# Kernel optimization log

Measured on AMD Instinct MI355X. Metric: run time of the kernel, lower is better.

## Reference

```python
import jax, jax.numpy as jnp
import numpy as np

LAM = 0.5  # self.lam_
N, T, C, H, W = 8, 8, 128, 64, 64


def setup_inputs() -> dict:
    key = jax.random.key(0)
    k1, k2, k3, k4 = jax.random.split(key, 4)
    x = jax.random.normal(k1, (N, T, C, H, W), dtype=jnp.float32)
    # Conv2d(2,1,k=3,p=1,bias=False) weights: [out=1, in=2, 3, 3]
    w_conv1 = jax.random.normal(k2, (1, 2, 3, 3), dtype=jnp.float32) * 0.1
    w_conv2 = jax.random.normal(k3, (1, 2, 3, 3), dtype=jnp.float32) * 0.1
    # Conv3d(2T, T, k=3, p=1, bias=False): [out=T, in=2T, 3, 3, 3]
    w_conv_last = jax.random.normal(k4, (T, 2 * T, 3, 3, 3), dtype=jnp.float32) * 0.05
    return {"x": x, "w_conv1": w_conv1, "w_conv2": w_conv2, "w_conv_last": w_conv_last}


def _conv2d_same(y, wgt):
    # y: [B, 2, H, W], wgt: [1, 2, 3, 3] -> [B, 1, H, W]
    return jax.lax.conv_general_dilated(
        y, wgt, window_strides=(1, 1), padding=[(1, 1), (1, 1)],
        dimension_numbers=("NCHW", "OIHW", "NCHW"))


def reference(x, w_conv1, w_conv2, w_conv_last):
    n, t, c, h, w = x.shape
    kc = int(c * LAM)
    kt = int(t * LAM)

    # pooled importance map: avg + max over spatial -> [n, t, c]
    M = jnp.mean(x, axis=(3, 4)) + jnp.max(x, axis=(3, 4))

    # --- channel top-k mask ---
    # Faithful to the torch fancy-index scatter loop: important_channels[:, i, topk_[:, i]] = 1
    # broadcasts the write over ALL batch rows, i.e. a per-timestep union over the batch.
    _, topk_c = jax.lax.top_k(M, kc)                                  # [n, t, kc]
    t_ids = jnp.broadcast_to(jnp.arange(t)[None, :, None], topk_c.shape)
    mask_ch = jnp.zeros((t, c), x.dtype).at[t_ids.ravel(), topk_c.ravel()].set(1.0)  # [t, c]

    # --- time top-k mask (on transposed map) ---
    _, topk_t = jax.lax.top_k(jnp.swapaxes(M, 1, 2), kt)              # [n, c, kt]
    c_ids = jnp.broadcast_to(jnp.arange(c)[None, :, None], topk_t.shape)
    mask_tm = jnp.zeros((c, t), x.dtype).at[c_ids.ravel(), topk_t.ravel()].set(1.0).T  # [t, c]

    # important iff (mask_ch + mask_tm)/2 == 0.5  <=> XOR of the two masks
    imp = jnp.where(mask_ch + mask_tm == 1.0, 1.0, 0.0).astype(x.dtype)  # [t, c]
    imp = imp[None, :, :, None, None]                                    # [1, t, c, 1, 1]

    im_feat = imp * x
    sub_feat = x - im_feat  # (1 - imp) * x

    im_avg = jnp.mean(im_feat, axis=2, keepdims=True) / LAM           # [n, t, 1, h, w]
    im_max = jnp.max(im_feat, axis=2, keepdims=True)
    sub_avg = jnp.mean(sub_feat, axis=2, keepdims=True) / (1.0 - LAM)
    sub_max = jnp.max(sub_feat, axis=2, keepdims=True)

    im_x = jnp.concatenate([im_avg, im_max], axis=2)                  # [n, t, 2, h, w]
    sub_x = jnp.concatenate([sub_avg, sub_max], axis=2)

    # SeqToANNContainer flattens (t, n) then conv2d per-sample; flatten order irrelevant.
    im_map = jax.nn.sigmoid(_conv2d_same(im_x.reshape(n * t, 2, h, w), w_conv1)).reshape(n, t, 1, h, w)
    sub_map = jax.nn.sigmoid(_conv2d_same(sub_x.reshape(n * t, 2, h, w), w_conv2)).reshape(n, t, 1, h, w)

    htsa = jnp.concatenate([im_map * im_feat, sub_map * sub_feat], axis=1)  # [n, 2t, c, h, w]

    # Conv3d(2t -> t, k=3, p=1): treats t as channels, c as depth
    out = jax.lax.conv_general_dilated(
        htsa, w_conv_last, window_strides=(1, 1, 1),
        padding=[(1, 1), (1, 1), (1, 1)],
        dimension_numbers=("NCDHW", "OIDHW", "NCDHW"))
    return out  # [n, t, c, h, w]
```

## Files before the change

### kernel.cpp

```cpp
#include <hip/hip_runtime.h>
#include <math.h>

#define NN 8
#define TT 8
#define CC 128
#define HH 64
#define WW 64
#define HW 4096

typedef unsigned int u32;
typedef unsigned short u16;
typedef __attribute__((ext_vector_type(8))) short short8;
typedef __attribute__((ext_vector_type(4))) float floatx4;

__device__ __forceinline__ u16 f2bf(float f){
    u32 u = __float_as_uint(f);
    u32 r = (u + 0x7fffu + ((u >> 16) & 1u)) >> 16;
    return (u16)r;
}
__device__ __forceinline__ float bf2f(u16 h){
    return __uint_as_float(((u32)h) << 16);
}

__global__ __launch_bounds__(256) void k1_M(const float* __restrict__ x, float* __restrict__ M){
    int plane = blockIdx.x * 4 + (threadIdx.x >> 6);
    int lane  = threadIdx.x & 63;
    const float* p = x + (size_t)plane * HW;
    float s = 0.f, mx = -INFINITY;
    #pragma unroll
    for (int it = 0; it < 16; ++it){
        float4 v = *(const float4*)(p + it*256 + lane*4);
        s += v.x + v.y + v.z + v.w;
        mx = fmaxf(mx, fmaxf(fmaxf(v.x, v.y), fmaxf(v.z, v.w)));
    }
    #pragma unroll
    for (int off = 32; off > 0; off >>= 1){
        s += __shfl_xor(s, off, 64);
        mx = fmaxf(mx, __shfl_xor(mx, off, 64));
    }
    if (lane == 0) M[plane] = s * (1.0f/(float)HW) + mx;
}

__global__ __launch_bounds__(128) void k2_imp(const float* __restrict__ M, float* __restrict__ imp){
    int t = blockIdx.x;
    int c = threadIdx.x;
    __shared__ float Ms[NN*CC];
    for (int n = 0; n < NN; ++n)
        Ms[n*CC + c] = M[(n*TT + t)*CC + c];
    __syncthreads();
    bool sel_ch = false;
    for (int n = 0; n < NN; ++n){
        float mv = Ms[n*CC + c];
        int rank = 0;
        for (int c2 = 0; c2 < CC; ++c2){
            float v2 = Ms[n*CC + c2];
            rank += (v2 > mv) || (v2 == mv && c2 < c);
        }
        sel_ch = sel_ch || (rank < 64);
    }
    bool sel_tm = false;
    for (int n = 0; n < NN; ++n){
        float mv = M[(n*TT + t)*CC + c];
        int rank = 0;
        for (int t2 = 0; t2 < TT; ++t2){
            float v2 = M[(n*TT + t2)*CC + c];
            rank += (v2 > mv) || (v2 == mv && t2 < t);
        }
        sel_tm = sel_tm || (rank < 4);
    }
    imp[t*CC + c] = (sel_ch != sel_tm) ? 1.0f : 0.0f;
}

__global__ __launch_bounds__(512) void k3a_stats(const float* __restrict__ x,
        const float* __restrict__ imp, u16* __restrict__ st){
    int nt = blockIdx.x; int t = nt & 7;
    int px = (blockIdx.y * 512 + threadIdx.x) * 4;
    __shared__ float ipr[CC];
    if (threadIdx.x < CC) ipr[threadIdx.x] = imp[t*CC + threadIdx.x];
    __syncthreads();
    const float* xp = x + (size_t)nt * CC * HW + px;
    float sa[4] = {0,0,0,0}, sb[4] = {0,0,0,0};
    float ma[4] = {-INFINITY,-INFINITY,-INFINITY,-INFINITY};
    float mb[4] = {-INFINITY,-INFINITY,-INFINITY,-INFINITY};
    for (int c = 0; c < CC; ++c){
        float ip = ipr[c];
        float4 v = *(const float4*)(xp + (size_t)c*HW);
        float vv[4] = {v.x, v.y, v.z, v.w};
        #pragma unroll
        for (int j = 0; j < 4; ++j){
            float a = ip*vv[j], b = vv[j] - a;
            sa[j] += a; sb[j] += b;
            ma[j] = fmaxf(ma[j], a); mb[j] = fmaxf(mb[j], b);
        }
    }
    union { u16 h[4]; uint2 v2; } o;
    #pragma unroll
    for (int j = 0; j < 4; ++j) o.h[j] = f2bf(sa[j] * (1.f/64.f));
    *(uint2*)(st + (nt*4+0)*HW + px) = o.v2;
    #pragma unroll
    for (int j = 0; j < 4; ++j) o.h[j] = f2bf(ma[j]);
    *(uint2*)(st + (nt*4+1)*HW + px) = o.v2;
    #pragma unroll
    for (int j = 0; j < 4; ++j) o.h[j] = f2bf(sb[j] * (1.f/64.f));
    *(uint2*)(st + (nt*4+2)*HW + px) = o.v2;
    #pragma unroll
    for (int j = 0; j < 4; ++j) o.h[j] = f2bf(mb[j]);
    *(uint2*)(st + (nt*4+3)*HW + px) = o.v2;
}

__global__ __launch_bounds__(256) void k3b_maps(const u16* __restrict__ st,
        const float* __restrict__ w1, const float* __restrict__ w2,
        float* __restrict__ maps){
    int nt = blockIdx.x;
    int y0 = blockIdx.y * 16;
    __shared__ float S[4*18*66];
    int tid = threadIdx.x;
    for (int idx = tid; idx < 4*18*66; idx += 256){
        int s  = idx / 1188;
        int r  = (idx % 1188) / 66;
        int xx = idx % 66;
        int gy = y0 - 1 + r, gx = xx - 1;
        float v = 0.f;
        if ((u32)gy < HH && (u32)gx < WW)
            v = bf2f(st[(nt*4 + s)*HW + gy*WW + gx]);
        S[idx] = v;
    }
    __syncthreads();
    float wa[18], wb[18];
    #pragma unroll
    for (int i = 0; i < 18; ++i){ wa[i] = w1[i]; wb[i] = w2[i]; }
    for (int k = 0; k < 4; ++k){
        int p = k*256 + tid;
        int y = p >> 6, xx = p & 63;
        float zi = 0.f, zs = 0.f;
        #pragma unroll
        for (int dy = 0; dy < 3; ++dy)
            #pragma unroll
            for (int dx = 0; dx < 3; ++dx){
                int sp = (y+dy)*66 + xx + dx;
                zi += wa[dy*3+dx] * S[sp] + wa[9+dy*3+dx] * S[1188 + sp];
                zs += wb[dy*3+dx] * S[2376 + sp] + wb[9+dy*3+dx] * S[3564 + sp];
            }
        maps[(nt*2+0)*HW + y0*WW + p] = 1.0f / (1.0f + expf(-zi));
        maps[(nt*2+1)*HW + y0*WW + p] = 1.0f / (1.0f + expf(-zs));
    }
}

__global__ __launch_bounds__(64) void kW_frag(const float* __restrict__ wlast,
        const float* __restrict__ impf, u16* __restrict__ fw){
    int c_out = blockIdx.x;
    int stp   = blockIdx.y;
    int lane  = threadIdx.x;
    int m = lane & 15, q = lane >> 4;
    int tap = 4*stp + q;
    int dc = tap / 9;
    int c_in = c_out - 1 + dc;
    bool valid = (m < 8) && (tap < 27) && ((u32)c_in < CC);
    union { u16 h[8]; uint4 v; } pk;
    #pragma unroll
    for (int j = 0; j < 8; ++j){
        float wv = 0.f;
        if (valid){
            int idx = (impf[j*CC + c_in] > 0.f) ? j : j + 8;
            wv = wlast[(m*16 + idx)*27 + tap];
        }
        pk.h[j] = f2bf(wv);
    }
    *(uint4*)(fw + (((size_t)c_out*7 + stp)*64 + lane)*8) = pk.v;
}

constexpr int offb16(int tap){
    return (((tap/9)*6 + ((tap/3)%3))*66 + (tap%3))*16;
}

__global__ __launch_bounds__(256, 6) void k5_fuse(
        const float* __restrict__ x, const float* __restrict__ impf,
        const float* __restrict__ maps, const u16* __restrict__ fw,
        float* __restrict__ out){
    __shared__ __align__(16) u16 ft[1584*8];
    __shared__ u32 mofs[4][8];
    int tid  = threadIdx.x;
    int lane = tid & 63;
    int w    = tid >> 6;
    int c0 = blockIdx.x * 2;
    int y0 = blockIdx.y * 4;
    int n  = blockIdx.z;
    int cl = w & 1;
    int c_out = c0 + cl;

    if (tid < 32){
        int cc = tid >> 3, t = tid & 7;
        int gc = c0 - 1 + cc;
        float ip = ((u32)gc < CC) ? impf[t*CC + gc] : 0.f;
        mofs[cc][t] = (u32)(((n*TT + t)*2 + (ip > 0.f ? 0 : 1)) * HW);
    }

    short8 afr[7];
    const u16* fwb = fw + ((size_t)c_out*7*64 + lane)*8;
    #pragma unroll
    for (int stp = 0; stp < 7; ++stp)
        afr[stp] = *(const short8*)(fwb + stp*512);
    __syncthreads();

    for (int idx = tid; idx < 1584; idx += 256){
        int cc  = idx / 396;
        int rm  = idx % 396;
        int yyl = rm / 66;
        int xx  = rm % 66;
        int gc = c0 - 1 + cc;
        int gy = y0 - 1 + yyl;
        int gx = xx - 1;
        uint4 v = make_uint4(0,0,0,0);
        if ((u32)gc < CC && (u32)gy < HH && (u32)gx < WW){
            int gp = gy*WW + gx;
            const float* xn = x + ((size_t)(n*TT)*CC + gc)*HW + gp;
            const float* mb = maps + gp;
            u16 hv[8];
            #pragma unroll
            for (int t = 0; t < TT; ++t){
                float xv = xn[(size_t)t*CC*HW];
                float mv = mb[mofs[cc][t]];
                hv[t] = f2bf(xv * mv);
            }
            v.x = (u32)hv[0] | ((u32)hv[1] << 16);
            v.y = (u32)hv[2] | ((u32)hv[3] << 16);
            v.z = (u32)hv[4] | ((u32)hv[5] << 16);
            v.w = (u32)hv[6] | ((u32)hv[7] << 16);
        }
        *(uint4*)(ft + idx*8) = v;
    }
    __syncthreads();

    int col = lane & 15;
    int q   = lane >> 4;
    const char* fb = (const char*)ft;
    int offs[7];
    #pragma unroll
    for (int stp = 0; stp < 7; ++stp){
        int tap = 4*stp + q;
        if (tap >= 27) tap = 0;
        offs[stp] = offb16(tap);
    }
    for (int yy = 0; yy < 2; ++yy){
        int yl = (w >> 1)*2 + yy;
        int rowb = ((cl*6 + yl)*66 + col)*16;
        #pragma unroll
        for (int xp = 0; xp < 2; ++xp){
            int b0off = rowb + xp*512;
            int b1off = b0off + 256;
            floatx4 acc0 = {0.f,0.f,0.f,0.f};
            floatx4 acc1 = {0.f,0.f,0.f,0.f};
            #pragma unroll
            for (int stp = 0; stp < 7; ++stp){
                short8 b0 = *(const short8*)(fb + b0off + offs[stp]);
                short8 b1 = *(const short8*)(fb + b1off + offs[stp]);
                acc0 = __builtin_amdgcn_mfma_f32_16x16x32_bf16(afr[stp], b0, acc0, 0, 0, 0);
                acc1 = __builtin_amdgcn_mfma_f32_16x16x32_bf16(afr[stp], b1, acc1, 0, 0, 0);
            }
            if (lane < 32){
                int y = y0 + yl;
                int xa = xp*32 + col;
                #pragma unroll
                for (int rg = 0; rg < 4; ++rg){
                    int o = (lane >> 4)*4 + rg;
                    size_t ob = (((size_t)(n*TT + o))*CC + c_out)*HW + y*WW;
                    out[ob + xa]      = acc0[rg];
                    out[ob + xa + 16] = acc1[rg];
                }
            }
        }
    }
}

__global__ __launch_bounds__(256) void k5_conv3d(
        const float* __restrict__ x,
        const float* __restrict__ impf, const float* __restrict__ wlast,
        const float* __restrict__ maps, float* __restrict__ out){
    __shared__ __align__(16) u16 fim[1584*8];
    __shared__ __align__(16) u16 fsb[1584*8];
    __shared__ u32 maskw[CC*4];
    int tid  = threadIdx.x;
    int lane = tid & 63;
    int w    = tid >> 6;
    int c0 = blockIdx.x * 2;
    int y0 = blockIdx.y * 4;
    int n  = blockIdx.z;

    for (int idx = tid; idx < CC*4; idx += 256){
        int c = idx >> 2, j = idx & 3;
        u32 m = (impf[(2*j)*CC + c]   > 0.f ? 0x0000FFFFu : 0u)
              | (impf[(2*j+1)*CC + c] > 0.f ? 0xFFFF0000u : 0u);
        maskw[idx] = m;
    }

    for (int idx = tid; idx < 896; idx += 256){
        int stp = idx >> 6;
        int l   = idx & 63;
        int m = l & 15, q = l >> 4;
        int i0 = (q & 1) * 8, s = q >> 1;
        int tap = 2*stp + s;
        bool valid = (m < 8) && (tap < 27);
        union { u16 h[8]; uint4 v; } pk;
        #pragma unroll
        for (int j = 0; j < 8; ++j){
            float wv = valid ? wlast[(m*16 + i0 + j)*27 + tap] : 0.f;
            pk.h[j] = f2bf(wv);
        }
        *(uint4*)(fim + idx*8) = pk.v;
    }
    __syncthreads();
    short8 afr[14];
    #pragma unroll
    for (int stp = 0; stp < 14; ++stp)
        afr[stp] = *(const short8*)(fim + (stp*64 + lane)*8);
    __syncthreads();

    for (int idx = tid; idx < 1584; idx += 256){
        int cc  = idx / 396;
        int rm  = idx % 396;
        int yyl = rm / 66;
        int xx  = rm % 66;
        int gc = c0 - 1 + cc;
        int gy = y0 - 1 + yyl;
        int gx = xx - 1;
        uint4 vim = make_uint4(0,0,0,0), vsb = make_uint4(0,0,0,0);
        if ((u32)gc < CC && (u32)gy < HH && (u32)gx < WW){
            int gp = gy*WW + gx;
            u32 al[4];
            const float* xn  = x    + ((size_t)(n*TT)*CC + gc)*HW + gp;
            const float* mpn = maps + ((size_t)n*TT*2)*HW + gp;
            u16 hv[8];
            #pragma unroll
            for (int t = 0; t < TT; ++t){
                float ip = impf[t*CC + gc];
                float xv = xn[(size_t)t*CC*HW];
                float mv = mpn[((size_t)t*2 + (ip > 0.f ? 0 : 1))*HW];
                hv[t] = f2bf(xv * mv);
            }
            #pragma unroll
            for (int j = 0; j < 4; ++j)
                al[j] = (u32)hv[2*j] | ((u32)hv[2*j+1] << 16);
            u32 m0 = maskw[gc*4+0], m1 = maskw[gc*4+1];
            u32 m2 = maskw[gc*4+2], m3 = maskw[gc*4+3];
            vim.x = al[0] & m0; vim.y = al[1] & m1;
            vim.z = al[2] & m2; vim.w = al[3] & m3;
            vsb.x = al[0] ^ vim.x; vsb.y = al[1] ^ vim.y;
            vsb.z = al[2] ^ vim.z; vsb.w = al[3] ^ vim.w;
        }
        *(uint4*)(fim + idx*8) = vim;
        *(uint4*)(fsb + idx*8) = vsb;
    }
    __syncthreads();

    int col = lane & 15;
    int q   = (lane >> 4) & 1;
    int s   = lane >> 5;
    const char* fb = (const char*)(q ? fsb : fim);
    int offs[14];
    #pragma unroll
    for (int stp = 0; stp < 14; ++stp){
        int tap = 2*stp + s;
        if (tap >= 27) tap = 0;
        offs[stp] = offb16(tap);
    }
    int cl = w & 1;
    for (int yy = 0; yy < 2; ++yy){
        int yl = (w >> 1)*2 + yy;
        int rowb = ((cl*6 + yl)*66 + col)*16;
        #pragma unroll
        for (int xp = 0; xp < 2; ++xp){
            int b0off = rowb + xp*512;
            int b1off = b0off + 256;
            floatx4 acc0 = {0.f,0.f,0.f,0.f};
            floatx4 acc1 = {0.f,0.f,0.f,0.f};
            #pragma unroll
            for (int stp = 0; stp < 14; ++stp){
                short8 b0 = *(const short8*)(fb + b0off + offs[stp]);
                short8 b1 = *(const short8*)(fb + b1off + offs[stp]);
                acc0 = __builtin_amdgcn_mfma_f32_16x16x32_bf16(afr[stp], b0, acc0, 0, 0, 0);
                acc1 = __builtin_amdgcn_mfma_f32_16x16x32_bf16(afr[stp], b1, acc1, 0, 0, 0);
            }
            if (lane < 32){
                int c = c0 + cl, y = y0 + yl;
                int xa = xp*32 + col;
                #pragma unroll
                for (int rg = 0; rg < 4; ++rg){
                    int o = (lane >> 4)*4 + rg;
                    size_t ob = (((size_t)(n*TT + o))*CC + c)*HW + y*WW;
                    out[ob + xa]      = acc0[rg];
                    out[ob + xa + 16] = acc1[rg];
                }
            }
        }
    }
}

extern "C" void kernel_launch(void* const* d_in, const int* in_sizes, int n_in,
                              void* d_out, int out_size, void* d_ws, size_t ws_size,
                              hipStream_t stream){
    const float* x     = (const float*)d_in[0];
    const float* w1    = (const float*)d_in[1];
    const float* w2    = (const float*)d_in[2];
    const float* wlast = (const float*)d_in[3];
    float* out = (float*)d_out;

    float* ws   = (float*)d_ws;
    float* M    = ws;
    float* imp  = ws + 8192;
    float* maps = ws + 9216;
    u16*   st   = (u16*)(ws + 9216 + 524288);
    u16*   fw   = st;
    const size_t WS_MAIN = (size_t)(9216 + 524288 + 524288) * 4;

    k1_M      <<<dim3(NN*TT*CC/4), dim3(256), 0, stream>>>(x, M);
    k2_imp    <<<dim3(TT),         dim3(128), 0, stream>>>(M, imp);
    k3a_stats <<<dim3(NN*TT, 2),   dim3(512), 0, stream>>>(x, imp, st);
    k3b_maps  <<<dim3(NN*TT, 4),   dim3(256), 0, stream>>>(st, w1, w2, maps);
    if (ws_size >= WS_MAIN){
        kW_frag <<<dim3(CC, 7), dim3(64), 0, stream>>>(wlast, imp, fw);
        k5_fuse <<<dim3(CC/2, HH/4, NN), dim3(256), 0, stream>>>(x, imp, maps, fw, out);
    } else {
        k5_conv3d <<<dim3(CC/2, HH/4, NN), dim3(256), 0, stream>>>(x, imp, wlast, maps, out);
    }
}
```

Baseline: 349.2 us.

## Vectorize conv3d output stores via swapped MFMA operands; split stats kernel into more blocks

The fused conv3d kernel swaps the MFMA A/B operands so each lane holds four consecutive x outputs for one output channel. Those are written as float4 stores, replacing scalar stores. The stats kernel goes from 128 blocks of 512 threads to 512 blocks of 128 threads, and its channel loop is unrolled by four to batch loads. The aim is better store coalescing and more parallelism and memory-level parallelism in the stats pass. In exchange, half the lanes in the conv kernel stay idle during the store, and the operand swap must keep the fragment layout correct.

```diff
diff --git a/kernel.cpp b/kernel.cpp
--- a/kernel.cpp
+++ b/kernel.cpp
@@ -71,26 +71,33 @@
     imp[t*CC + c] = (sel_ch != sel_tm) ? 1.0f : 0.0f;
 }
 
-__global__ __launch_bounds__(512) void k3a_stats(const float* __restrict__ x,
+__global__ __launch_bounds__(128) void k3a_stats(const float* __restrict__ x,
         const float* __restrict__ imp, u16* __restrict__ st){
     int nt = blockIdx.x; int t = nt & 7;
-    int px = (blockIdx.y * 512 + threadIdx.x) * 4;
+    int px = (blockIdx.y * 128 + threadIdx.x) * 4;
     __shared__ float ipr[CC];
-    if (threadIdx.x < CC) ipr[threadIdx.x] = imp[t*CC + threadIdx.x];
+    ipr[threadIdx.x] = imp[t*CC + threadIdx.x];
     __syncthreads();
     const float* xp = x + (size_t)nt * CC * HW + px;
     float sa[4] = {0,0,0,0}, sb[4] = {0,0,0,0};
     float ma[4] = {-INFINITY,-INFINITY,-INFINITY,-INFINITY};
     float mb[4] = {-INFINITY,-INFINITY,-INFINITY,-INFINITY};
-    for (int c = 0; c < CC; ++c){
-        float ip = ipr[c];
-        float4 v = *(const float4*)(xp + (size_t)c*HW);
-        float vv[4] = {v.x, v.y, v.z, v.w};
-        #pragma unroll
-        for (int j = 0; j < 4; ++j){
-            float a = ip*vv[j], b = vv[j] - a;
-            sa[j] += a; sb[j] += b;
-            ma[j] = fmaxf(ma[j], a); mb[j] = fmaxf(mb[j], b);
+    for (int c = 0; c < CC; c += 4){
+        float4 v[4]; float ip[4];
+        #pragma unroll
+        for (int k = 0; k < 4; ++k){
+            v[k]  = *(const float4*)(xp + (size_t)(c+k)*HW);
+            ip[k] = ipr[c+k];
+        }
+        #pragma unroll
+        for (int k = 0; k < 4; ++k){
+            float vv[4] = {v[k].x, v[k].y, v[k].z, v[k].w};
+            #pragma unroll
+            for (int j = 0; j < 4; ++j){
+                float a = ip[k]*vv[j], b = vv[j] - a;
+                sa[j] += a; sb[j] += b;
+                ma[j] = fmaxf(ma[j], a); mb[j] = fmaxf(mb[j], b);
+            }
         }
     }
     union { u16 h[4]; uint2 v2; } o;
@@ -241,9 +248,13 @@
         if (tap >= 27) tap = 0;
         offs[stp] = offb16(tap);
     }
+    int o = lane & 15;
+    bool ostore = (o < 8);
+    size_t obase = (((size_t)(n*TT + (o & 7)))*CC + c_out)*HW;
     for (int yy = 0; yy < 2; ++yy){
         int yl = (w >> 1)*2 + yy;
         int rowb = ((cl*6 + yl)*66 + col)*16;
+        int y = y0 + yl;
         #pragma unroll
         for (int xp = 0; xp < 2; ++xp){
             int b0off = rowb + xp*512;
@@ -254,19 +265,14 @@
             for (int stp = 0; stp < 7; ++stp){
                 short8 b0 = *(const short8*)(fb + b0off + offs[stp]);
                 short8 b1 = *(const short8*)(fb + b1off + offs[stp]);
-                acc0 = __builtin_amdgcn_mfma_f32_16x16x32_bf16(afr[stp], b0, acc0, 0, 0, 0);
-                acc1 = __builtin_amdgcn_mfma_f32_16x16x32_bf16(afr[stp], b1, acc1, 0, 0, 0);
-            }
-            if (lane < 32){
-                int y = y0 + yl;
-                int xa = xp*32 + col;
-                #pragma unroll
-                for (int rg = 0; rg < 4; ++rg){
-                    int o = (lane >> 4)*4 + rg;
-                    size_t ob = (((size_t)(n*TT + o))*CC + c_out)*HW + y*WW;
-                    out[ob + xa]      = acc0[rg];
-                    out[ob + xa + 16] = acc1[rg];
-                }
+                acc0 = __builtin_amdgcn_mfma_f32_16x16x32_bf16(b0, afr[stp], acc0, 0, 0, 0);
+                acc1 = __builtin_amdgcn_mfma_f32_16x16x32_bf16(b1, afr[stp], acc1, 0, 0, 0);
+            }
+            if (ostore){
+                int xa = xp*32 + (lane >> 4)*4;
+                size_t ob = obase + (size_t)y*WW + xa;
+                *(float4*)(out + ob)      = *(const float4*)&acc0;
+                *(float4*)(out + ob + 16) = *(const float4*)&acc1;
             }
         }
     }
@@ -414,7 +420,7 @@
 
     k1_M      <<<dim3(NN*TT*CC/4), dim3(256), 0, stream>>>(x, M);
     k2_imp    <<<dim3(TT),         dim3(128), 0, stream>>>(M, imp);
-    k3a_stats <<<dim3(NN*TT, 2),   dim3(512), 0, stream>>>(x, imp, st);
+    k3a_stats <<<dim3(NN*TT, 8),   dim3(128), 0, stream>>>(x, imp, st);
     k3b_maps  <<<dim3(NN*TT, 4),   dim3(256), 0, stream>>>(st, w1, w2, maps);
     if (ws_size >= WS_MAIN){
         kW_frag <<<dim3(CC, 7), dim3(64), 0, stream>>>(wlast, imp, fw);
```

Result: no change. 355.4 us (+1.8%).
